# Kernel tuning notes

Measured on AMD Instinct MI355X. Metric: run time of the kernel, lower is better.

The kernel has to match this reference:

```python
import jax, jax.numpy as jnp
import numpy as np

B, T, E, H = 16, 1024, 1024, 16
DH = E // H  # 64, divisible by 4
THETA = 10000.0


def setup_inputs() -> dict:
    key = jax.random.key(0)
    ks = jax.random.split(key, 10)
    inp = {
        "hidden_states": jax.random.normal(ks[0], (B, T, E), dtype=jnp.float32),
        "rope_pos": jax.random.randint(ks[1], (B, T, 2), 0, 32, dtype=jnp.int32),
    }
    s = 0.02
    inp["Wq"] = jax.random.normal(ks[2], (E, E), dtype=jnp.float32) * s
    inp["bq"] = jnp.zeros((E,), dtype=jnp.float32)
    inp["Wk"] = jax.random.normal(ks[3], (E, E), dtype=jnp.float32) * s
    inp["bk"] = jnp.zeros((E,), dtype=jnp.float32)
    inp["Wv"] = jax.random.normal(ks[4], (E, E), dtype=jnp.float32) * s
    inp["bv"] = jnp.zeros((E,), dtype=jnp.float32)
    inp["Wo"] = jax.random.normal(ks[5], (E, E), dtype=jnp.float32) * s
    inp["bo"] = jnp.zeros((E,), dtype=jnp.float32)
    return inp


def _rotate_half(x):
    # interleaved pairs: (x0,x1,x2,x3,...) -> (-x1,x0,-x3,x2,...)
    x_even = x[..., ::2]
    x_odd = x[..., 1::2]
    return jnp.stack((-x_odd, x_even), axis=-1).reshape(x.shape)


def _apply_rope_2d(q, k, rope_pos, theta):
    Dh = q.shape[-1]
    half, quarter = Dh // 2, Dh // 4
    dtype = q.dtype
    idx = jnp.arange(quarter, dtype=dtype)
    inv = (theta ** (-2.0 * idx / quarter)).astype(dtype)  # [quarter]
    pos_h = rope_pos[..., 0].astype(dtype)[..., None]  # [B,T,1]
    pos_w = rope_pos[..., 1].astype(dtype)[..., None]
    ang_h = pos_h * inv  # [B,T,quarter]
    ang_w = pos_w * inv
    ri = lambda a: jnp.repeat(a, 2, axis=-1)[:, None]  # -> [B,1,T,half]
    cos_h, sin_h = ri(jnp.cos(ang_h)), ri(jnp.sin(ang_h))
    cos_w, sin_w = ri(jnp.cos(ang_w)), ri(jnp.sin(ang_w))
    q_h, q_w = q[..., :half], q[..., half:]
    k_h, k_w = k[..., :half], k[..., half:]
    q_h = q_h * cos_h + _rotate_half(q_h) * sin_h
    k_h = k_h * cos_h + _rotate_half(k_h) * sin_h
    q_w = q_w * cos_w + _rotate_half(q_w) * sin_w
    k_w = k_w * cos_w + _rotate_half(k_w) * sin_w
    return jnp.concatenate([q_h, q_w], axis=-1), jnp.concatenate([k_h, k_w], axis=-1)


def reference(hidden_states, rope_pos, Wq, bq, Wk, bk, Wv, bv, Wo, bo):
    b, t, e = hidden_states.shape
    scale = DH ** -0.5
    # torch nn.Linear: y = x @ W.T + b, W is [out, in]
    proj = lambda x, W, bias: jnp.einsum('bte,oe->bto', x, W) + bias
    q = proj(hidden_states, Wq, bq).reshape(b, t, H, DH).transpose(0, 2, 1, 3)
    k = proj(hidden_states, Wk, bk).reshape(b, t, H, DH).transpose(0, 2, 1, 3)
    v = proj(hidden_states, Wv, bv).reshape(b, t, H, DH).transpose(0, 2, 1, 3)
    q, k = _apply_rope_2d(q, k, rope_pos, THETA)
    # eager attention: scores in input dtype, softmax in float32
    scores = jnp.einsum('bhqd,bhkd->bhqk', q, k) * scale
    w = jax.nn.softmax(scores.astype(jnp.float32), axis=-1).astype(q.dtype)
    out = jnp.einsum('bhqk,bhkd->bhqd', w, v)
    out = out.transpose(0, 2, 1, 3).reshape(b, t, e)
    return jnp.einsum('bte,oe->bto', out, Wo) + bo
```

## Files before the change

kernel.cpp:

```cpp
#include <hip/hip_runtime.h>
#include <hip/hip_bf16.h>

#define B_  16
#define T_  1024
#define E_  1024
#define H_  16
#define DH_ 64

typedef short s16x8 __attribute__((ext_vector_type(8)));
typedef float f32x4 __attribute__((ext_vector_type(4)));
typedef unsigned short u16x4 __attribute__((ext_vector_type(4)));

__device__ __forceinline__ void async_cp16(const void* g, void* l) {
  __builtin_amdgcn_global_load_lds(
      (__attribute__((address_space(1))) unsigned int*)(g),
      (__attribute__((address_space(3))) unsigned int*)(l), 16, 0, 0);
}

__device__ __forceinline__ s16x8 frag8(const void* p) { return *(const s16x8*)p; }

__device__ __forceinline__ float fexp2(float x) {
#if __has_builtin(__builtin_amdgcn_exp2f)
  return __builtin_amdgcn_exp2f(x);
#else
  return exp2f(x);
#endif
}

__device__ __forceinline__ unsigned short f2bu(float x) {
  __hip_bfloat16 h = __float2bfloat16(x);
  return *reinterpret_cast<unsigned short*>(&h);
}

__device__ __forceinline__ float bu2f(unsigned short u) {
  __hip_bfloat16 h = *reinterpret_cast<__hip_bfloat16*>(&u);
  return __bfloat162float(h);
}

__global__ __launch_bounds__(256) void cast_f32_bf16(const float* __restrict__ in,
                                                     __hip_bfloat16* __restrict__ out,
                                                     int n4) {
  int i = blockIdx.x * 256 + threadIdx.x;
  if (i >= n4) return;
  float4 v = ((const float4*)in)[i];
  u16x4 pk = {f2bu(v.x), f2bu(v.y), f2bu(v.z), f2bu(v.w)};
  *(u16x4*)(out + (size_t)i * 4) = pk;
}

#define G8_ISSUE(SRC_, LOFF_, H_, D_, KT_)                                      \
  {                                                                             \
    _Pragma("unroll") for (int u_ = 0; u_ < 2; ++u_) {                          \
      const int ch_ = u_ * 8 + wave;                                            \
      async_cp16(SRC_ + (size_t)((H_)*128 + ch_ * 8) * 2048 + (KT_)*128,        \
                 smem + (D_)*65536 + (LOFF_) + (H_)*16384 + ch_ * 1024);        \
    }                                                                           \
  }

#define G8_READ_A(D_, S_)                                                       \
  {                                                                             \
    _Pragma("unroll") for (int i_ = 0; i_ < 4; ++i_) {                          \
      const char* rp_ = smem + (D_)*65536 + wrow * 16384 +                      \
                        ((S_)*64 + i_ * 16 + col) * 128;                        \
      af[i_][0] = frag8(rp_ + sw0);                                             \
      af[i_][1] = frag8(rp_ + sw1);                                             \
    }                                                                           \
  }

#define G8_READ_B(D_, T8_, BF_)                                                 \
  {                                                                             \
    _Pragma("unroll") for (int j_ = 0; j_ < 2; ++j_) {                          \
      const char* rp_ = smem + (D_)*65536 + 32768 + (wcol >> 1) * 16384 +       \
                        ((wcol & 1) * 64 + (T8_)*32 + j_ * 16 + col) * 128;     \
      BF_[j_][0] = frag8(rp_ + sw0);                                            \
      BF_[j_][1] = frag8(rp_ + sw1);                                            \
    }                                                                           \
  }

#define G8_MFMA(S_, T8_, BF_)                                                   \
  {                                                                             \
    __builtin_amdgcn_s_setprio(1);                                              \
    _Pragma("unroll") for (int i_ = 0; i_ < 4; ++i_)                            \
      _Pragma("unroll") for (int j_ = 0; j_ < 2; ++j_) {                        \
        acc[(S_)*4 + i_][(T8_)*2 + j_] = __builtin_amdgcn_mfma_f32_16x16x32_bf16( \
            af[i_][0], BF_[j_][0], acc[(S_)*4 + i_][(T8_)*2 + j_], 0, 0, 0);    \
        acc[(S_)*4 + i_][(T8_)*2 + j_] = __builtin_amdgcn_mfma_f32_16x16x32_bf16( \
            af[i_][1], BF_[j_][1], acc[(S_)*4 + i_][(T8_)*2 + j_], 0, 0, 0);    \
      }                                                                         \
    __builtin_amdgcn_s_setprio(0);                                              \
  }

#define G8_KTILE(D_, GA_, GB_, KTA_, KTB_, VM_)                                 \
  G8_READ_A(D_, 0)                                                              \
  G8_READ_B(D_, 0, bf0)                                                         \
  if (GA_) G8_ISSUE(Asrc, 0, 0, (D_) ^ 1, KTA_)                                 \
  __builtin_amdgcn_s_barrier();                                                 \
  G8_MFMA(0, 0, bf0)                                                            \
  __builtin_amdgcn_s_barrier();                                                 \
  G8_READ_B(D_, 1, bf1)                                                         \
  if (GA_) G8_ISSUE(Asrc, 0, 1, (D_) ^ 1, KTA_)                                 \
  __builtin_amdgcn_s_barrier();                                                 \
  G8_MFMA(0, 1, bf1)                                                            \
  __builtin_amdgcn_s_barrier();                                                 \
  G8_READ_A(D_, 1)                                                              \
  if (GB_) G8_ISSUE(Bsrc, 32768, 0, (D_), KTB_)                                 \
  __builtin_amdgcn_s_barrier();                                                 \
  G8_MFMA(1, 1, bf1)                                                            \
  __builtin_amdgcn_s_barrier();                                                 \
  if (GB_) G8_ISSUE(Bsrc, 32768, 1, (D_), KTB_)                                 \
  __builtin_amdgcn_s_barrier();                                                 \
  G8_MFMA(1, 0, bf0)                                                            \
  if (VM_) { asm volatile("s_waitcnt vmcnt(4)" ::: "memory"); }                 \
  else     { asm volatile("s_waitcnt vmcnt(0)" ::: "memory"); }                 \
  __builtin_amdgcn_s_barrier();

#define G8_CORE(APTR_, BPTR_)                                                   \
  __shared__ __align__(16) char smem[131072];                                   \
  const int tid = threadIdx.x;                                                  \
  const int lane = tid & 63, wave = tid >> 6;                                   \
  const int col = lane & 15, quad = lane >> 4;                                  \
  const int wrow = wave >> 2, wcol = wave & 3;                                  \
  const int r8 = lane >> 3;                                                     \
  const int gsw = (lane & 7) ^ r8;                                              \
  const int sw0 = (quad ^ (col & 7)) * 16;                                      \
  const int sw1 = ((quad + 4) ^ (col & 7)) * 16;                                \
  const char* Asrc = (const char*)(APTR_) + (size_t)(bm + r8) * 2048 + gsw * 16;\
  const char* Bsrc = (const char*)(BPTR_) + (size_t)(bn + r8) * 2048 + gsw * 16;\
  const f32x4 fzero = {0.f, 0.f, 0.f, 0.f};                                     \
  f32x4 acc[8][4];                                                              \
  _Pragma("unroll") for (int i_ = 0; i_ < 8; i_++)                              \
    _Pragma("unroll") for (int j_ = 0; j_ < 4; j_++) acc[i_][j_] = fzero;       \
  s16x8 af[4][2], bf0[2][2], bf1[2][2];                                         \
  G8_ISSUE(Bsrc, 32768, 0, 0, 0)                                                \
  G8_ISSUE(Bsrc, 32768, 1, 0, 0)                                                \
  G8_ISSUE(Asrc, 0, 0, 0, 0)                                                    \
  G8_ISSUE(Asrc, 0, 1, 0, 0)                                                    \
  G8_ISSUE(Bsrc, 32768, 0, 1, 1)                                                \
  G8_ISSUE(Bsrc, 32768, 1, 1, 1)                                                \
  asm volatile("s_waitcnt vmcnt(4)" ::: "memory");                              \
  __builtin_amdgcn_s_barrier();                                                 \
  _Pragma("clang loop unroll(disable)") for (int it = 0; it < 8; ++it) {        \
    const bool g7 = (it < 7);                                                   \
    G8_KTILE(0, true, g7, 2 * it + 1, 2 * it + 2, g7)                           \
    G8_KTILE(1, g7, g7, 2 * it + 2, 2 * it + 3, g7)                             \
  }

__global__ __launch_bounds__(512, 2) void gemm_qkv(const __hip_bfloat16* __restrict__ A,
                                                   const __hip_bfloat16* __restrict__ Wqkv,
                                                   const float* __restrict__ bq,
                                                   const float* __restrict__ bk,
                                                   const float* __restrict__ bv,
                                                   __hip_bfloat16* __restrict__ Qb,
                                                   __hip_bfloat16* __restrict__ Kb,
                                                   __hip_bfloat16* __restrict__ Vt) {
  const int wg = (blockIdx.x & 7) * 96 + (blockIdx.x >> 3);
  const int bm = (wg & 63) << 8;
  const int bn = (wg >> 6) << 8;
  G8_CORE(A, Wqkv)

  const int seg = bn >> 10;
  const float* bp = (seg == 0) ? bq : (seg == 1) ? bk : bv;
  const int nbase = (bn & 1023) + wcol * 64;
  float bcol[4];
#pragma unroll
  for (int j = 0; j < 4; j++) bcol[j] = bp[nbase + j * 16 + col];
  if (seg < 2) {
    __hip_bfloat16* P = (seg == 0) ? Qb : Kb;
#pragma unroll
    for (int mi = 0; mi < 8; mi++) {
      const int gr0 = bm + wrow * 128 + mi * 16 + quad * 4;
#pragma unroll
      for (int ni = 0; ni < 4; ni++) {
        const int nc = nbase + ni * 16 + col;
#pragma unroll
        for (int r = 0; r < 4; r++)
          P[(size_t)(gr0 + r) * 1024 + nc] = __float2bfloat16(acc[mi][ni][r] + bcol[ni]);
      }
    }
  } else {
#pragma unroll
    for (int mi = 0; mi < 8; mi++) {
      const int gr0 = bm + wrow * 128 + mi * 16 + quad * 4;
      const int bb = gr0 >> 10, tt = gr0 & 1023;
#pragma unroll
      for (int ni = 0; ni < 4; ni++) {
        const int nc = nbase + ni * 16 + col;
        const int hh = nc >> 6, dd = nc & 63;
        u16x4 pk = {f2bu(acc[mi][ni][0] + bcol[ni]), f2bu(acc[mi][ni][1] + bcol[ni]),
                    f2bu(acc[mi][ni][2] + bcol[ni]), f2bu(acc[mi][ni][3] + bcol[ni])};
        *(u16x4*)(Vt + (((size_t)bb * H_ + hh) * DH_ + dd) * T_ + tt) = pk;
      }
    }
  }
}

__global__ __launch_bounds__(512, 2) void gemm_out(const __hip_bfloat16* __restrict__ A,
                                                   const __hip_bfloat16* __restrict__ Bw,
                                                   const float* __restrict__ bias,
                                                   float* __restrict__ Cout) {
  const int wg = (blockIdx.x & 7) * 32 + (blockIdx.x >> 3);
  const int bm = (wg & 63) << 8;
  const int bn = (wg >> 6) << 8;
  G8_CORE(A, Bw)

  const int nbase = bn + wcol * 64;
  float bcol[4];
#pragma unroll
  for (int j = 0; j < 4; j++) bcol[j] = bias[nbase + j * 16 + col];
#pragma unroll
  for (int mi = 0; mi < 8; mi++) {
    const int gr0 = bm + wrow * 128 + mi * 16 + quad * 4;
#pragma unroll
    for (int ni = 0; ni < 4; ni++) {
      const int gcol = nbase + ni * 16 + col;
#pragma unroll
      for (int r = 0; r < 4; r++)
        Cout[(size_t)(gr0 + r) * 1024 + gcol] = acc[mi][ni][r] + bcol[ni];
    }
  }
}

__global__ __launch_bounds__(256) void rope2d(__hip_bfloat16* __restrict__ Q,
                                              __hip_bfloat16* __restrict__ K,
                                              const int* __restrict__ pos) {
  const int row = blockIdx.x;
  const int t   = threadIdx.x;
  const float ph = (float)pos[row * 2 + 0];
  const float pw = (float)pos[row * 2 + 1];
  const int pd = (2 * t) & 31;
  float cs[2], sn[2];
#pragma unroll
  for (int i = 0; i < 2; i++) {
    int pdi = pd + i;
    int f = pdi & 15;
    float p = (pdi & 16) ? pw : ph;
    float inv = __expf((float)f * (-1.1512925464970229f));
    float ang = p * inv;
    __sincosf(ang, &sn[i], &cs[i]);
  }
  const float QSC = 0.18033688011112043f;
  size_t base = (size_t)row * E_ + 4 * t;
  {
    u16x4 q4 = *(u16x4*)(Q + base);
    float e0 = bu2f(q4[0]), e1 = bu2f(q4[1]), e2 = bu2f(q4[2]), e3 = bu2f(q4[3]);
    u16x4 o4 = {f2bu((e0 * cs[0] - e1 * sn[0]) * QSC),
                f2bu((e1 * cs[0] + e0 * sn[0]) * QSC),
                f2bu((e2 * cs[1] - e3 * sn[1]) * QSC),
                f2bu((e3 * cs[1] + e2 * sn[1]) * QSC)};
    *(u16x4*)(Q + base) = o4;
  }
  {
    u16x4 k4 = *(u16x4*)(K + base);
    float e0 = bu2f(k4[0]), e1 = bu2f(k4[1]), e2 = bu2f(k4[2]), e3 = bu2f(k4[3]);
    u16x4 o4 = {f2bu(e0 * cs[0] - e1 * sn[0]),
                f2bu(e1 * cs[0] + e0 * sn[0]),
                f2bu(e2 * cs[1] - e3 * sn[1]),
                f2bu(e3 * cs[1] + e2 * sn[1])};
    *(u16x4*)(K + base) = o4;
  }
}

__global__ __launch_bounds__(256, 3) void attn_flash(const __hip_bfloat16* __restrict__ Q,
                                                     const __hip_bfloat16* __restrict__ Kt,
                                                     const __hip_bfloat16* __restrict__ Vt,
                                                     __hip_bfloat16* __restrict__ Oa) {
  __shared__ __align__(16) __hip_bfloat16 QP[128 * 72];
  __shared__ __align__(16) __hip_bfloat16 Ks[64 * 72];
  __shared__ __align__(16) __hip_bfloat16 Vs[64 * 72];

  const int bid = blockIdx.x;
  const int bh = bid >> 3;
  const int b = bh >> 4, h = bh & 15;
  const int qt = bid & 7;
  const int tid = threadIdx.x;
  const int lane = tid & 63, wave = tid >> 6;
  const int col = lane & 15, quad = lane >> 4;

  const size_t qrow0 = (size_t)b * T_ + qt * 128;

#pragma unroll
  for (int cc = 0; cc < 4; ++cc) {
    int c = tid + cc * 256;
    int r = c >> 3, k8 = c & 7;
    const float4* src = (const float4*)((const char*)(Q + (qrow0 + r) * E_ + h * DH_)) + k8;
    *(float4*)((char*)QP + r * 144 + k8 * 16) = *src;
  }

  const f32x4 fzero = {0.f, 0.f, 0.f, 0.f};
  f32x4 o[2][4];
  float lr[2] = {0.f, 0.f};
#pragma unroll
  for (int g = 0; g < 2; g++)
#pragma unroll
    for (int j = 0; j < 4; j++) o[g][j] = fzero;
  s16x8 qf[2][2];
  char* Pw = (char*)QP + wave * 32 * 144;

  for (int kt2 = 0; kt2 < 16; ++kt2) {
    __syncthreads();
    const int kb = kt2 * 64;
#pragma unroll
    for (int cc = 0; cc < 4; ++cc) {
      int c = tid + cc * 256;
      if (c < 512) {
        int r = c >> 3, k8 = c & 7;
        const float4* src = (const float4*)((const char*)(Kt + ((size_t)b * T_ + kb + r) * E_ + h * DH_)) + k8;
        *(float4*)((char*)Ks + r * 144 + k8 * 16) = *src;
      } else {
        int c2 = c - 512;
        int d = c2 >> 3, k8 = c2 & 7;
        const float4* src = (const float4*)((const char*)(Vt + (((size_t)b * H_ + h) * DH_ + d) * T_ + kb)) + k8;
        *(float4*)((char*)Vs + d * 144 + k8 * 16) = *src;
      }
    }
    __syncthreads();
    if (kt2 == 0) {
#pragma unroll
      for (int g = 0; g < 2; g++) {
        qf[g][0] = frag8((const char*)QP + (g * 64 + wave * 16 + col) * 144 + quad * 16);
        qf[g][1] = frag8((const char*)QP + (g * 64 + wave * 16 + col) * 144 + 64 + quad * 16);
      }
      __syncthreads();
    }
    s16x8 kf[4][2];
#pragma unroll
    for (int ktile = 0; ktile < 4; ktile++) {
      kf[ktile][0] = frag8((const char*)Ks + (ktile * 16 + col) * 144 + quad * 16);
      kf[ktile][1] = frag8((const char*)Ks + (ktile * 16 + col) * 144 + 64 + quad * 16);
    }
#pragma unroll
    for (int g = 0; g < 2; g++) {
#pragma unroll
      for (int ktile = 0; ktile < 4; ktile++) {
        f32x4 d = fzero;
        d = __builtin_amdgcn_mfma_f32_16x16x32_bf16(kf[ktile][0], qf[g][0], d, 0, 0, 0);
        d = __builtin_amdgcn_mfma_f32_16x16x32_bf16(kf[ktile][1], qf[g][1], d, 0, 0, 0);
        float p0 = fexp2(d[0]), p1 = fexp2(d[1]), p2 = fexp2(d[2]), p3 = fexp2(d[3]);
        lr[g] += (p0 + p1) + (p2 + p3);
        u16x4 pk = {f2bu(p0), f2bu(p1), f2bu(p2), f2bu(p3)};
        *(u16x4*)(Pw + (g * 16 + col) * 144 + ktile * 32 + quad * 8) = pk;
      }
    }
    s16x8 vf[4][2];
#pragma unroll
    for (int jm = 0; jm < 4; jm++) {
      vf[jm][0] = frag8((const char*)Vs + (jm * 16 + col) * 144 + quad * 16);
      vf[jm][1] = frag8((const char*)Vs + (jm * 16 + col) * 144 + 64 + quad * 16);
    }
#pragma unroll
    for (int g = 0; g < 2; g++) {
      s16x8 pf0 = frag8(Pw + (g * 16 + col) * 144 + quad * 16);
      s16x8 pf1 = frag8(Pw + (g * 16 + col) * 144 + 64 + quad * 16);
#pragma unroll
      for (int jm = 0; jm < 4; jm++) {
        o[g][jm] = __builtin_amdgcn_mfma_f32_16x16x32_bf16(vf[jm][0], pf0, o[g][jm], 0, 0, 0);
        o[g][jm] = __builtin_amdgcn_mfma_f32_16x16x32_bf16(vf[jm][1], pf1, o[g][jm], 0, 0, 0);
      }
    }
  }
#pragma unroll
  for (int g = 0; g < 2; g++) {
    lr[g] += __shfl_xor(lr[g], 16, 64);
    lr[g] += __shfl_xor(lr[g], 32, 64);
  }
#pragma unroll
  for (int g = 0; g < 2; g++) {
    float invl = 1.f / lr[g];
    size_t grow = qrow0 + g * 64 + wave * 16 + col;
    char* obase = (char*)(Oa + grow * E_ + h * DH_);
#pragma unroll
    for (int jm = 0; jm < 4; jm++) {
      u16x4 pk = {f2bu(o[g][jm][0] * invl), f2bu(o[g][jm][1] * invl),
                  f2bu(o[g][jm][2] * invl), f2bu(o[g][jm][3] * invl)};
      *(u16x4*)(obase + jm * 32 + quad * 8) = pk;
    }
  }
}

extern "C" void kernel_launch(void* const* d_in, const int* in_sizes, int n_in,
                              void* d_out, int out_size, void* d_ws, size_t ws_size,
                              hipStream_t stream) {
  const float* X   = (const float*)d_in[0];
  const int*   pos = (const int*)d_in[1];
  const float* Wq  = (const float*)d_in[2];
  const float* bq  = (const float*)d_in[3];
  const float* Wk  = (const float*)d_in[4];
  const float* bk  = (const float*)d_in[5];
  const float* Wv  = (const float*)d_in[6];
  const float* bv  = (const float*)d_in[7];
  const float* Wo  = (const float*)d_in[8];
  const float* bo  = (const float*)d_in[9];
  float* out = (float*)d_out;

  char* ws = (char*)d_ws;
  const size_t MB = 1024 * 1024;
  __hip_bfloat16* Xb    = (__hip_bfloat16*)(ws + 0 * MB);
  __hip_bfloat16* Qb    = (__hip_bfloat16*)(ws + 32 * MB);
  __hip_bfloat16* Kb    = (__hip_bfloat16*)(ws + 64 * MB);
  __hip_bfloat16* Vtb   = (__hip_bfloat16*)(ws + 96 * MB);
  __hip_bfloat16* Wqkvb = (__hip_bfloat16*)(ws + 128 * MB);
  __hip_bfloat16* Wob   = (__hip_bfloat16*)(ws + 136 * MB);
  __hip_bfloat16* Ab    = Xb;

  cast_f32_bf16<<<16384, 256, 0, stream>>>(X,  Xb,  4194304);
  cast_f32_bf16<<<1024,  256, 0, stream>>>(Wq, Wqkvb,           262144);
  cast_f32_bf16<<<1024,  256, 0, stream>>>(Wk, Wqkvb + 1048576, 262144);
  cast_f32_bf16<<<1024,  256, 0, stream>>>(Wv, Wqkvb + 2097152, 262144);
  cast_f32_bf16<<<1024,  256, 0, stream>>>(Wo, Wob,             262144);

  gemm_qkv<<<768, 512, 0, stream>>>(Xb, Wqkvb, bq, bk, bv, Qb, Kb, Vtb);

  rope2d<<<16384, 256, 0, stream>>>(Qb, Kb, pos);
  attn_flash<<<2048, 256, 0, stream>>>(Qb, Kb, Vtb, Ab);

  gemm_out<<<256, 512, 0, stream>>>(Ab, Wob, bo, out);
}
```

Measured before the change: 446.7 us.

## Fuse casts into one launch, fold RoPE into QKV GEMM, prefetch attention K/V

Merges the five cast launches into a single kernel. Applies 2D RoPE and the Q scale inside the QKV GEMM epilogue, using a shared-memory cos/sin table and a lane shuffle, which removes the separate rope2d read/write pass over Q and K. In the attention kernel, block IDs are remapped so each XCD handles contiguous heads, and the next K/V tile is register-prefetched while the current one is computed. The risks are extra epilogue work and shuffles in the GEMM, plus higher register pressure in attention.

After: 433.8 us. 1.03x faster.

```diff
diff --git a/kernel.cpp b/kernel.cpp
--- a/kernel.cpp
+++ b/kernel.cpp
@@ -37,14 +37,30 @@
   return __bfloat162float(h);
 }
 
-__global__ __launch_bounds__(256) void cast_f32_bf16(const float* __restrict__ in,
-                                                     __hip_bfloat16* __restrict__ out,
-                                                     int n4) {
-  int i = blockIdx.x * 256 + threadIdx.x;
-  if (i >= n4) return;
-  float4 v = ((const float4*)in)[i];
+__global__ __launch_bounds__(256) void cast_all(const float* __restrict__ X,
+                                                const float* __restrict__ Wq,
+                                                const float* __restrict__ Wk,
+                                                const float* __restrict__ Wv,
+                                                const float* __restrict__ Wo,
+                                                __hip_bfloat16* __restrict__ Xb,
+                                                __hip_bfloat16* __restrict__ Wqkvb,
+                                                __hip_bfloat16* __restrict__ Wob) {
+  const int bid = blockIdx.x;
+  const float* src;
+  __hip_bfloat16* dst;
+  int i;
+  if (bid < 16384) {
+    src = X; dst = Xb; i = bid * 256 + threadIdx.x;
+  } else {
+    const int wb = bid - 16384;
+    const int w = wb >> 10;
+    src = (w == 0) ? Wq : (w == 1) ? Wk : (w == 2) ? Wv : Wo;
+    dst = (w == 3) ? Wob : Wqkvb + (size_t)w * 1048576;
+    i = (wb & 1023) * 256 + threadIdx.x;
+  }
+  float4 v = ((const float4*)src)[i];
   u16x4 pk = {f2bu(v.x), f2bu(v.y), f2bu(v.z), f2bu(v.w)};
-  *(u16x4*)(out + (size_t)i * 4) = pk;
+  *(u16x4*)(dst + (size_t)i * 4) = pk;
 }
 
 #define G8_ISSUE(SRC_, LOFF_, H_, D_, KT_)                                      \
@@ -149,6 +165,7 @@
                                                    const float* __restrict__ bq,
                                                    const float* __restrict__ bk,
                                                    const float* __restrict__ bv,
+                                                   const int* __restrict__ pos,
                                                    __hip_bfloat16* __restrict__ Qb,
                                                    __hip_bfloat16* __restrict__ Kb,
                                                    __hip_bfloat16* __restrict__ Vt) {
@@ -164,16 +181,37 @@
 #pragma unroll
   for (int j = 0; j < 4; j++) bcol[j] = bp[nbase + j * 16 + col];
   if (seg < 2) {
+    __syncthreads();
+    float2* tab = (float2*)smem;
+    {
+      const int p_ = tid >> 4, f_ = tid & 15;
+      const float inv = __expf((float)f_ * -1.1512925464970229f);
+      float s_, c_;
+      __sincosf((float)p_ * inv, &s_, &c_);
+      tab[tid] = make_float2(c_, s_);
+    }
+    __syncthreads();
+    const float SCL = (seg == 0) ? 0.18033688011112043f : 1.0f;
     __hip_bfloat16* P = (seg == 0) ? Qb : Kb;
+    const int codd = col & 1;
 #pragma unroll
     for (int mi = 0; mi < 8; mi++) {
       const int gr0 = bm + wrow * 128 + mi * 16 + quad * 4;
 #pragma unroll
-      for (int ni = 0; ni < 4; ni++) {
-        const int nc = nbase + ni * 16 + col;
-#pragma unroll
-        for (int r = 0; r < 4; r++)
-          P[(size_t)(gr0 + r) * 1024 + nc] = __float2bfloat16(acc[mi][ni][r] + bcol[ni]);
+      for (int r = 0; r < 4; r++) {
+        const int grow = gr0 + r;
+        const int iph = pos[grow * 2 + 0];
+        const int ipw = pos[grow * 2 + 1];
+#pragma unroll
+        for (int ni = 0; ni < 4; ni++) {
+          const int f = ((ni & 1) << 3) + (col >> 1);
+          const int p_ = (ni >= 2) ? ipw : iph;
+          const float2 cs = tab[p_ * 16 + f];
+          const float v = acc[mi][ni][r] + bcol[ni];
+          const float vp = __shfl_xor(v, 1, 64);
+          const float rot = codd ? (v * cs.x + vp * cs.y) : (v * cs.x - vp * cs.y);
+          P[(size_t)grow * 1024 + nbase + ni * 16 + col] = __float2bfloat16(rot * SCL);
+        }
       }
     }
   } else {
@@ -219,46 +257,6 @@
   }
 }
 
-__global__ __launch_bounds__(256) void rope2d(__hip_bfloat16* __restrict__ Q,
-                                              __hip_bfloat16* __restrict__ K,
-                                              const int* __restrict__ pos) {
-  const int row = blockIdx.x;
-  const int t   = threadIdx.x;
-  const float ph = (float)pos[row * 2 + 0];
-  const float pw = (float)pos[row * 2 + 1];
-  const int pd = (2 * t) & 31;
-  float cs[2], sn[2];
-#pragma unroll
-  for (int i = 0; i < 2; i++) {
-    int pdi = pd + i;
-    int f = pdi & 15;
-    float p = (pdi & 16) ? pw : ph;
-    float inv = __expf((float)f * (-1.1512925464970229f));
-    float ang = p * inv;
-    __sincosf(ang, &sn[i], &cs[i]);
-  }
-  const float QSC = 0.18033688011112043f;
-  size_t base = (size_t)row * E_ + 4 * t;
-  {
-    u16x4 q4 = *(u16x4*)(Q + base);
-    float e0 = bu2f(q4[0]), e1 = bu2f(q4[1]), e2 = bu2f(q4[2]), e3 = bu2f(q4[3]);
-    u16x4 o4 = {f2bu((e0 * cs[0] - e1 * sn[0]) * QSC),
-                f2bu((e1 * cs[0] + e0 * sn[0]) * QSC),
-                f2bu((e2 * cs[1] - e3 * sn[1]) * QSC),
-                f2bu((e3 * cs[1] + e2 * sn[1]) * QSC)};
-    *(u16x4*)(Q + base) = o4;
-  }
-  {
-    u16x4 k4 = *(u16x4*)(K + base);
-    float e0 = bu2f(k4[0]), e1 = bu2f(k4[1]), e2 = bu2f(k4[2]), e3 = bu2f(k4[3]);
-    u16x4 o4 = {f2bu(e0 * cs[0] - e1 * sn[0]),
-                f2bu(e1 * cs[0] + e0 * sn[0]),
-                f2bu(e2 * cs[1] - e3 * sn[1]),
-                f2bu(e3 * cs[1] + e2 * sn[1])};
-    *(u16x4*)(K + base) = o4;
-  }
-}
-
 __global__ __launch_bounds__(256, 3) void attn_flash(const __hip_bfloat16* __restrict__ Q,
                                                      const __hip_bfloat16* __restrict__ Kt,
                                                      const __hip_bfloat16* __restrict__ Vt,
@@ -268,9 +266,10 @@
   __shared__ __align__(16) __hip_bfloat16 Vs[64 * 72];
 
   const int bid = blockIdx.x;
-  const int bh = bid >> 3;
+  const int xcd = bid & 7, slot = bid >> 3;
+  const int bh = xcd * 32 + (slot >> 3);
+  const int qt = slot & 7;
   const int b = bh >> 4, h = bh & 15;
-  const int qt = bid & 7;
   const int tid = threadIdx.x;
   const int lane = tid & 63, wave = tid >> 6;
   const int col = lane & 15, quad = lane >> 4;
@@ -285,6 +284,25 @@
     *(float4*)((char*)QP + r * 144 + k8 * 16) = *src;
   }
 
+  const char* Ksrc = (const char*)(Kt + (size_t)b * T_ * E_ + h * DH_);
+  const char* Vsrc = (const char*)(Vt + ((size_t)b * H_ + h) * DH_ * (size_t)T_);
+  const int sr = tid >> 3, sk8 = tid & 7;
+  float4 kv[4];
+#define LOADKV(KB_)                                                                  \
+  {                                                                                  \
+    kv[0] = *(const float4*)(Ksrc + (size_t)((KB_) + sr) * 2048 + sk8 * 16);         \
+    kv[1] = *(const float4*)(Ksrc + (size_t)((KB_) + 32 + sr) * 2048 + sk8 * 16);    \
+    kv[2] = *(const float4*)(Vsrc + (size_t)sr * 2048 + (KB_)*2 + sk8 * 16);         \
+    kv[3] = *(const float4*)(Vsrc + (size_t)(32 + sr) * 2048 + (KB_)*2 + sk8 * 16);  \
+  }
+#define WRITEKV()                                                                    \
+  {                                                                                  \
+    *(float4*)((char*)Ks + sr * 144 + sk8 * 16) = kv[0];                             \
+    *(float4*)((char*)Ks + (32 + sr) * 144 + sk8 * 16) = kv[1];                      \
+    *(float4*)((char*)Vs + sr * 144 + sk8 * 16) = kv[2];                             \
+    *(float4*)((char*)Vs + (32 + sr) * 144 + sk8 * 16) = kv[3];                      \
+  }
+
   const f32x4 fzero = {0.f, 0.f, 0.f, 0.f};
   f32x4 o[2][4];
   float lr[2] = {0.f, 0.f};
@@ -295,23 +313,10 @@
   s16x8 qf[2][2];
   char* Pw = (char*)QP + wave * 32 * 144;
 
+  LOADKV(0)
   for (int kt2 = 0; kt2 < 16; ++kt2) {
     __syncthreads();
-    const int kb = kt2 * 64;
-#pragma unroll
-    for (int cc = 0; cc < 4; ++cc) {
-      int c = tid + cc * 256;
-      if (c < 512) {
-        int r = c >> 3, k8 = c & 7;
-        const float4* src = (const float4*)((const char*)(Kt + ((size_t)b * T_ + kb + r) * E_ + h * DH_)) + k8;
-        *(float4*)((char*)Ks + r * 144 + k8 * 16) = *src;
-      } else {
-        int c2 = c - 512;
-        int d = c2 >> 3, k8 = c2 & 7;
-        const float4* src = (const float4*)((const char*)(Vt + (((size_t)b * H_ + h) * DH_ + d) * T_ + kb)) + k8;
-        *(float4*)((char*)Vs + d * 144 + k8 * 16) = *src;
-      }
-    }
+    WRITEKV()
     __syncthreads();
     if (kt2 == 0) {
 #pragma unroll
@@ -321,6 +326,7 @@
       }
       __syncthreads();
     }
+    if (kt2 < 15) LOADKV((kt2 + 1) * 64)
     s16x8 kf[4][2];
 #pragma unroll
     for (int ktile = 0; ktile < 4; ktile++) {
@@ -357,6 +363,8 @@
       }
     }
   }
+#undef LOADKV
+#undef WRITEKV
 #pragma unroll
   for (int g = 0; g < 2; g++) {
     lr[g] += __shfl_xor(lr[g], 16, 64);
@@ -401,15 +409,10 @@
   __hip_bfloat16* Wob   = (__hip_bfloat16*)(ws + 136 * MB);
   __hip_bfloat16* Ab    = Xb;
 
-  cast_f32_bf16<<<16384, 256, 0, stream>>>(X,  Xb,  4194304);
-  cast_f32_bf16<<<1024,  256, 0, stream>>>(Wq, Wqkvb,           262144);
-  cast_f32_bf16<<<1024,  256, 0, stream>>>(Wk, Wqkvb + 1048576, 262144);
-  cast_f32_bf16<<<1024,  256, 0, stream>>>(Wv, Wqkvb + 2097152, 262144);
-  cast_f32_bf16<<<1024,  256, 0, stream>>>(Wo, Wob,             262144);
-
-  gemm_qkv<<<768, 512, 0, stream>>>(Xb, Wqkvb, bq, bk, bv, Qb, Kb, Vtb);
-
-  rope2d<<<16384, 256, 0, stream>>>(Qb, Kb, pos);
+  cast_all<<<20480, 256, 0, stream>>>(X, Wq, Wk, Wv, Wo, Xb, Wqkvb, Wob);
+
+  gemm_qkv<<<768, 512, 0, stream>>>(Xb, Wqkvb, bq, bk, bv, pos, Qb, Kb, Vtb);
+
   attn_flash<<<2048, 256, 0, stream>>>(Qb, Kb, Vtb, Ab);
 
   gemm_out<<<256, 512, 0, stream>>>(Ab, Wob, bo, out);
```
